# Kernel optimization log

Hardware: AMD Instinct MI355X
Metric: run time of the kernel (lower is better)

Reference implementation:

```python
import jax, jax.numpy as jnp
import numpy as np

B, M, N, D, NH, DH = 2, 2048, 2048, 1024, 16, 64
STD = 0.02

def setup_inputs() -> dict:
    key = jax.random.key(0)
    ks = jax.random.split(key, 7)
    query = jax.random.normal(ks[0], (B, M, D), dtype=jnp.float32)
    key_value = jax.random.normal(ks[1], (B, N, D), dtype=jnp.float32)
    key_padding_mask = jax.random.uniform(ks[2], (B, N)) < 0.1
    # torch Linear weight is (out,in); store as (in,out) for x @ W
    W_Q = STD * jax.random.truncated_normal(ks[3], -2.0, 2.0, (D, NH * DH), dtype=jnp.float32)
    W_K = STD * jax.random.truncated_normal(ks[4], -2.0, 2.0, (D, NH * DH), dtype=jnp.float32)
    W_V = STD * jax.random.truncated_normal(ks[5], -2.0, 2.0, (D, NH * DH), dtype=jnp.float32)
    W_O = STD * jax.random.truncated_normal(ks[6], -2.0, 2.0, (NH * DH, D), dtype=jnp.float32)
    return {"query": query, "key_value": key_value, "key_padding_mask": key_padding_mask,
            "W_Q": W_Q, "W_K": W_K, "W_V": W_V, "W_O": W_O}

def reference(query, key_value, key_padding_mask, W_Q, W_K, W_V, W_O):
    scale = 1.0 / jnp.sqrt(jnp.float32(DH))
    Q = (query @ W_Q).reshape(B, M, NH, DH)       # (B,M,H,dh)
    K = (key_value @ W_K).reshape(B, N, NH, DH)   # (B,N,H,dh)
    V = (key_value @ W_V).reshape(B, N, NH, DH)
    scores = jnp.einsum('bmhd,bnhd->bhmn', Q, K) * scale  # (B,H,M,N)
    scores = jnp.where(key_padding_mask[:, None, None, :], -jnp.inf, scores)
    attn = jax.nn.softmax(scores, axis=-1)
    out = jnp.einsum('bhmn,bnhd->bmhd', attn, V).reshape(B, M, NH * DH)
    return out @ W_O
```

## Files before the change

### kernel.cpp

```cpp
#include <hip/hip_runtime.h>
#include <math.h>

#define BB 2
#define SEQ 2048
#define DMODEL 1024
#define NHH 16
#define DHH 64

typedef __bf16 bf16;
typedef __attribute__((ext_vector_type(8))) __bf16 bf16x8;
typedef __attribute__((ext_vector_type(4))) float f32x4;

#define C1f 0.18033688011112042f
#define C2f -5.770780163555854f

__global__ __launch_bounds__(256) void cvt2_bf16(const float* __restrict__ in0,
                                                 bf16* __restrict__ out0,
                                                 const float* __restrict__ in1,
                                                 bf16* __restrict__ out1, int n8) {
  int i = blockIdx.x * 256 + threadIdx.x;
  if (i >= n8) return;
  const float* in = blockIdx.y ? in1 : in0;
  bf16* out = blockIdx.y ? out1 : out0;
  const float4* p = (const float4*)in + 2 * (size_t)i;
  float4 a = p[0], b = p[1];
  bf16x8 v;
  v[0] = (bf16)a.x; v[1] = (bf16)a.y; v[2] = (bf16)a.z; v[3] = (bf16)a.w;
  v[4] = (bf16)b.x; v[5] = (bf16)b.y; v[6] = (bf16)b.z; v[7] = (bf16)b.w;
  *((bf16x8*)out + i) = v;
}

__global__ __launch_bounds__(256) void wt_cvt(const float* __restrict__ W0, const float* __restrict__ W1,
                                              const float* __restrict__ W2, const float* __restrict__ W3,
                                              bf16* __restrict__ O0, bf16* __restrict__ O1,
                                              bf16* __restrict__ O2, bf16* __restrict__ O3) {
  __shared__ bf16 T[64][72];
  const float* W; bf16* O;
  switch (blockIdx.z) {
    case 0: W = W0; O = O0; break;
    case 1: W = W1; O = O1; break;
    case 2: W = W2; O = O2; break;
    default: W = W3; O = O3; break;
  }
  const int n0 = blockIdx.x * 64, k0 = blockIdx.y * 64;
  const int t = threadIdx.x;
  {
    int k = t >> 2, ns = (t & 3) * 16;
    const float* g = W + (size_t)(k0 + k) * DMODEL + n0 + ns;
#pragma unroll
    for (int q = 0; q < 4; ++q) {
      float4 f = *(const float4*)(g + 4 * q);
      T[ns + 4 * q + 0][k] = (bf16)f.x;
      T[ns + 4 * q + 1][k] = (bf16)f.y;
      T[ns + 4 * q + 2][k] = (bf16)f.z;
      T[ns + 4 * q + 3][k] = (bf16)f.w;
    }
  }
  __syncthreads();
  {
    int n = t >> 2, ks = (t & 3) * 16;
    bf16x8 a = *(const bf16x8*)&T[n][ks];
    bf16x8 b = *(const bf16x8*)&T[n][ks + 8];
    bf16* o = O + (size_t)(n0 + n) * DMODEL + k0 + ks;
    *(bf16x8*)o = a;
    *(bf16x8*)(o + 8) = b;
  }
}

template <bool F32OUT>
__device__ __forceinline__ void gemm64_body(const bf16* __restrict__ A,
                                            const bf16* __restrict__ Bt,
                                            float* __restrict__ Cf,
                                            bf16* __restrict__ Cb,
                                            bf16* As, bf16* Bs) {
  const int t = threadIdx.x;
  const int lane = t & 63, wave = t >> 6;
  const int l15 = lane & 15, quad = lane >> 4;
  const int bm = blockIdx.y * 64, bn = blockIdx.x * 128;
  const int wr = wave >> 1, wc = wave & 1;

  const int srow = t >> 3;
  const int slot = t & 7;
  const int schunk = slot ^ (srow & 7);
  const bf16* gA = A + (size_t)(bm + srow) * DMODEL + schunk * 8;
  const bf16* gB = Bt + (size_t)(bn + srow) * DMODEL + schunk * 8;
  const int soff = srow * 64 + slot * 8;

  bf16x8 areg[2][2], breg[2][4];
#pragma unroll
  for (int s = 0; s < 2; ++s) {
#pragma unroll
    for (int j = 0; j < 2; ++j)
      areg[s][j] = *(const bf16x8*)(gA + (size_t)(32 * j) * DMODEL + s * 64);
#pragma unroll
    for (int j = 0; j < 4; ++j)
      breg[s][j] = *(const bf16x8*)(gB + (size_t)(32 * j) * DMODEL + s * 64);
  }

  f32x4 acc[2][4] = {};

#pragma unroll
  for (int it = 0; it < 16; ++it) {
    const int sel = it & 1;
    __syncthreads();
#pragma unroll
    for (int j = 0; j < 2; ++j) *(bf16x8*)&As[j * 2048 + soff] = areg[sel][j];
#pragma unroll
    for (int j = 0; j < 4; ++j) *(bf16x8*)&Bs[j * 2048 + soff] = breg[sel][j];
    __syncthreads();
    if (it + 2 < 16) {
      const int kn = (it + 2) * 64;
#pragma unroll
      for (int j = 0; j < 2; ++j)
        areg[sel][j] = *(const bf16x8*)(gA + (size_t)(32 * j) * DMODEL + kn);
#pragma unroll
      for (int j = 0; j < 4; ++j)
        breg[sel][j] = *(const bf16x8*)(gB + (size_t)(32 * j) * DMODEL + kn);
    }
#pragma unroll
    for (int ks = 0; ks < 2; ++ks) {
      bf16x8 af[2], bfr[4];
#pragma unroll
      for (int mt = 0; mt < 2; ++mt) {
        int row = wr * 32 + mt * 16 + l15;
        int s = (ks * 4 + quad) ^ (row & 7);
        af[mt] = *(const bf16x8*)&As[row * 64 + s * 8];
      }
#pragma unroll
      for (int nt = 0; nt < 4; ++nt) {
        int row = wc * 64 + nt * 16 + l15;
        int s = (ks * 4 + quad) ^ (row & 7);
        bfr[nt] = *(const bf16x8*)&Bs[row * 64 + s * 8];
      }
#pragma unroll
      for (int mt = 0; mt < 2; ++mt)
#pragma unroll
        for (int nt = 0; nt < 4; ++nt)
          acc[mt][nt] = __builtin_amdgcn_mfma_f32_16x16x32_bf16(af[mt], bfr[nt], acc[mt][nt], 0, 0, 0);
    }
  }

#pragma unroll
  for (int mt = 0; mt < 2; ++mt)
#pragma unroll
    for (int nt = 0; nt < 4; ++nt)
#pragma unroll
      for (int r = 0; r < 4; ++r) {
        int row = bm + wr * 32 + mt * 16 + quad * 4 + r;
        int col = bn + wc * 64 + nt * 16 + l15;
        if (F32OUT) Cf[(size_t)row * DMODEL + col] = acc[mt][nt][r];
        else Cb[(size_t)row * DMODEL + col] = (bf16)acc[mt][nt][r];
      }
}

__global__ __launch_bounds__(256) void gemm_qkv(const bf16* __restrict__ qbf,
                                                const bf16* __restrict__ kvbf,
                                                const bf16* __restrict__ WtQ,
                                                const bf16* __restrict__ WtK,
                                                const bf16* __restrict__ WtV,
                                                bf16* __restrict__ Qb,
                                                bf16* __restrict__ Kb,
                                                bf16* __restrict__ Vb) {
  __shared__ bf16 As[64 * 64];
  __shared__ bf16 Bs[128 * 64];
  const bf16 *A, *Bt; bf16* C;
  switch (blockIdx.z) {
    case 0: A = qbf; Bt = WtQ; C = Qb; break;
    case 1: A = kvbf; Bt = WtK; C = Kb; break;
    default: A = kvbf; Bt = WtV; C = Vb; break;
  }
  gemm64_body<false>(A, Bt, nullptr, C, As, Bs);
}

__global__ __launch_bounds__(256) void gemm_out(const bf16* __restrict__ A,
                                                const bf16* __restrict__ Wt,
                                                float* __restrict__ C) {
  __shared__ bf16 As[64 * 64];
  __shared__ bf16 Bs[128 * 64];
  gemm64_body<true>(A, Wt, C, nullptr, As, Bs);
}

__global__ __launch_bounds__(256) void attn_mfma(const bf16* __restrict__ Qb,
                                                 const bf16* __restrict__ Kb,
                                                 const bf16* __restrict__ Vb,
                                                 const int* __restrict__ maskp,
                                                 bf16* __restrict__ Ob) {
  __shared__ bf16 Ks[2][64 * 64];
  __shared__ bf16 Vt[2][64][68];
  __shared__ bf16 Ps[4][32][36];
  __shared__ bf16 msk01[2][64];

  const int blk = blockIdx.x;
  const int h = blk & 15;
  const int b = (blk >> 4) & 1;
  const int qb = blk >> 5;
  const int t = threadIdx.x;
  const int wave = t >> 6, lane = t & 63;
  const int l15 = lane & 15, quad = lane >> 4;
  bf16(*PsW)[36] = Ps[wave];

  const int kr = t >> 2, kq = t & 3;
  const bf16* gK = Kb + (size_t)(b * SEQ + kr) * DMODEL + h * 64 + kq * 16;
  const int s0 = (kq * 2) ^ (kr & 7), s1 = (kq * 2 + 1) ^ (kr & 7);
  const int nv = (t & 31) * 2, dc = (t >> 5) * 8;
  const bf16* gV = Vb + (size_t)(b * SEQ + nv) * DMODEL + h * 64 + dc;
  const int* gM = maskp + b * SEQ;

  {
    bf16x8 k0 = *(const bf16x8*)(gK);
    bf16x8 k1 = *(const bf16x8*)(gK + 8);
    bf16x8 v0 = *(const bf16x8*)(gV);
    bf16x8 v1 = *(const bf16x8*)(gV + DMODEL);
    int2 m2 = *(const int2*)(gM + nv);
    *(bf16x8*)&Ks[0][kr * 64 + s0 * 8] = k0;
    *(bf16x8*)&Ks[0][kr * 64 + s1 * 8] = k1;
    union U { bf16x8 v; uint32_t dw[4]; } a, c;
    a.v = v0; c.v = v1;
    const uint32_t zA = m2.x ? 0u : 0xFFFFFFFFu;
    const uint32_t zB = m2.y ? 0u : 0xFFFFFFFFu;
#pragma unroll
    for (int d2 = 0; d2 < 4; ++d2) {
      uint32_t A0 = a.dw[d2] & zA, B0 = c.dw[d2] & zB;
      *(uint32_t*)&Vt[0][dc + 2 * d2 + 0][nv] = __builtin_amdgcn_perm(B0, A0, 0x05040100u);
      *(uint32_t*)&Vt[0][dc + 2 * d2 + 1][nv] = __builtin_amdgcn_perm(B0, A0, 0x07060302u);
    }
    if (t < 64) msk01[0][t] = gM[t] ? (bf16)0.f : (bf16)1.f;
  }

  bf16x8 qf[2][2];
#pragma unroll
  for (int mt = 0; mt < 2; ++mt)
#pragma unroll
    for (int ks = 0; ks < 2; ++ks) {
      const bf16* g = Qb + (size_t)(b * SEQ + qb * 128 + wave * 32 + mt * 16 + l15) * DMODEL +
                      h * 64 + ks * 32 + quad * 8;
      qf[mt][ks] = *(const bf16x8*)g;
    }

  f32x4 o[2][4] = {};
  f32x4 acc_l[2] = {};

  __syncthreads();

  for (int it = 0; it < SEQ / 64; ++it) {
    const int p = it & 1;
    const bool more = (it + 1) < SEQ / 64;
    bf16x8 kreg0, kreg1, vreg0, vreg1;
    int2 vm;
    int mreg = 0;
    if (more) {
      const int nn = (it + 1) * 64;
      const bf16* gK2 = gK + (size_t)nn * DMODEL;
      const bf16* gV2 = gV + (size_t)nn * DMODEL;
      kreg0 = *(const bf16x8*)(gK2);
      kreg1 = *(const bf16x8*)(gK2 + 8);
      vreg0 = *(const bf16x8*)(gV2);
      vreg1 = *(const bf16x8*)(gV2 + DMODEL);
      vm = *(const int2*)(gM + nn + nv);
      if (t < 64) mreg = gM[nn + t];
    }

    f32x4 s[2][4] = {};
#pragma unroll
    for (int ks = 0; ks < 2; ++ks) {
      bf16x8 kf[4];
#pragma unroll
      for (int nt = 0; nt < 4; ++nt) {
        int row = nt * 16 + l15;
        int sl = (ks * 4 + quad) ^ (row & 7);
        kf[nt] = *(const bf16x8*)&Ks[p][row * 64 + sl * 8];
      }
#pragma unroll
      for (int mt = 0; mt < 2; ++mt)
#pragma unroll
        for (int nt = 0; nt < 4; ++nt)
          s[mt][nt] = __builtin_amdgcn_mfma_f32_16x16x32_bf16(qf[mt][ks], kf[nt], s[mt][nt], 0, 0, 0);
    }

#pragma unroll
    for (int ks2 = 0; ks2 < 2; ++ks2) {
#pragma unroll
      for (int mt = 0; mt < 2; ++mt)
#pragma unroll
        for (int nt2 = 0; nt2 < 2; ++nt2)
#pragma unroll
          for (int r = 0; r < 4; ++r) {
            float pex = __builtin_amdgcn_exp2f(s[mt][ks2 * 2 + nt2][r] * C1f + C2f);
            PsW[mt * 16 + quad * 4 + r][nt2 * 16 + l15] = (bf16)pex;
          }
      bf16x8 pa[2], vb[4];
#pragma unroll
      for (int mt = 0; mt < 2; ++mt)
        pa[mt] = *(const bf16x8*)&PsW[mt * 16 + l15][quad * 8];
#pragma unroll
      for (int dt = 0; dt < 4; ++dt)
        vb[dt] = *(const bf16x8*)&Vt[p][dt * 16 + l15][ks2 * 32 + quad * 8];
      union OU { bf16x8 v; uint32_t dw[4]; } of;
      of.v = *(const bf16x8*)&msk01[p][ks2 * 32 + quad * 8];
      const uint32_t zc = (l15 == 0) ? 0xFFFFFFFFu : 0u;
#pragma unroll
      for (int d = 0; d < 4; ++d) of.dw[d] &= zc;
#pragma unroll
      for (int mt = 0; mt < 2; ++mt) {
#pragma unroll
        for (int dt = 0; dt < 4; ++dt)
          o[mt][dt] = __builtin_amdgcn_mfma_f32_16x16x32_bf16(pa[mt], vb[dt], o[mt][dt], 0, 0, 0);
        acc_l[mt] = __builtin_amdgcn_mfma_f32_16x16x32_bf16(pa[mt], of.v, acc_l[mt], 0, 0, 0);
      }
    }

    if (more) {
      const int q = 1 - p;
      *(bf16x8*)&Ks[q][kr * 64 + s0 * 8] = kreg0;
      *(bf16x8*)&Ks[q][kr * 64 + s1 * 8] = kreg1;
      union U { bf16x8 v; uint32_t dw[4]; } a, c;
      a.v = vreg0; c.v = vreg1;
      const uint32_t zA = vm.x ? 0u : 0xFFFFFFFFu;
      const uint32_t zB = vm.y ? 0u : 0xFFFFFFFFu;
#pragma unroll
      for (int d2 = 0; d2 < 4; ++d2) {
        uint32_t A0 = a.dw[d2] & zA, B0 = c.dw[d2] & zB;
        *(uint32_t*)&Vt[q][dc + 2 * d2 + 0][nv] = __builtin_amdgcn_perm(B0, A0, 0x05040100u);
        *(uint32_t*)&Vt[q][dc + 2 * d2 + 1][nv] = __builtin_amdgcn_perm(B0, A0, 0x07060302u);
      }
      if (t < 64) msk01[q][t] = mreg ? (bf16)0.f : (bf16)1.f;
    }
    __syncthreads();
  }

#pragma unroll
  for (int mt = 0; mt < 2; ++mt)
#pragma unroll
    for (int r = 0; r < 4; ++r) {
      float lv = __shfl(acc_l[mt][r], lane & 48);
      float inv = 1.f / lv;
      int row = b * SEQ + qb * 128 + wave * 32 + mt * 16 + quad * 4 + r;
#pragma unroll
      for (int dt = 0; dt < 4; ++dt) {
        int col = h * 64 + dt * 16 + l15;
        Ob[(size_t)row * DMODEL + col] = (bf16)(o[mt][dt][r] * inv);
      }
    }
}

extern "C" void kernel_launch(void* const* d_in, const int* in_sizes, int n_in,
                              void* d_out, int out_size, void* d_ws, size_t ws_size,
                              hipStream_t stream) {
  (void)in_sizes; (void)n_in; (void)out_size; (void)ws_size;
  const float* query = (const float*)d_in[0];
  const float* key_value = (const float*)d_in[1];
  const int* mask = (const int*)d_in[2];
  const float* W_Q = (const float*)d_in[3];
  const float* W_K = (const float*)d_in[4];
  const float* W_V = (const float*)d_in[5];
  const float* W_O = (const float*)d_in[6];
  float* out = (float*)d_out;

  const size_t TOK = (size_t)BB * SEQ;
  const size_t TE = TOK * DMODEL;
  char* w = (char*)d_ws;
  bf16* qbf = (bf16*)w;   w += TE * 2;
  bf16* kvbf = (bf16*)w;  w += TE * 2;
  bf16* WtQ = (bf16*)w;   w += (size_t)DMODEL * DMODEL * 2;
  bf16* WtK = (bf16*)w;   w += (size_t)DMODEL * DMODEL * 2;
  bf16* WtV = (bf16*)w;   w += (size_t)DMODEL * DMODEL * 2;
  bf16* WtO = (bf16*)w;   w += (size_t)DMODEL * DMODEL * 2;
  bf16* Qbuf = (bf16*)w;  w += TE * 2;
  bf16* Kbuf = (bf16*)w;  w += TE * 2;
  bf16* Vbuf = (bf16*)w;  w += TE * 2;
  bf16* Obuf = (bf16*)w;  w += TE * 2;

  cvt2_bf16<<<dim3(TE / 8 / 256, 2), 256, 0, stream>>>(query, qbf, key_value, kvbf, TE / 8);
  wt_cvt<<<dim3(16, 16, 4), 256, 0, stream>>>(W_Q, W_K, W_V, W_O, WtQ, WtK, WtV, WtO);

  gemm_qkv<<<dim3(DMODEL / 128, TOK / 64, 3), 256, 0, stream>>>(qbf, kvbf, WtQ, WtK, WtV,
                                                                Qbuf, Kbuf, Vbuf);

  attn_mfma<<<BB * NHH * (SEQ / 128), 256, 0, stream>>>(Qbuf, Kbuf, Vbuf, mask, Obuf);

  gemm_out<<<dim3(DMODEL / 128, TOK / 64), 256, 0, stream>>>(Obuf, WtO, out);
}
```

Baseline: 235.1 us.

## Use 8 waves per attention block, 16 query rows each, split K/V loading

The attention kernel now launches 512 threads per block instead of 256. Each of the 8 waves handles 16 query rows rather than 32, and the K-tile and V-tile prefetch work is split between the first four and last four waves. This roughly halves per-thread registers and work, aiming for more wave-level parallelism and better latency hiding. In exchange, every K/V tile loaded into LDS feeds half as many MFMAs per wave, and the larger block has more barrier overhead.

```diff
diff --git a/kernel.cpp b/kernel.cpp
--- a/kernel.cpp
+++ b/kernel.cpp
@@ -180,14 +180,14 @@
   gemm64_body<true>(A, Wt, C, nullptr, As, Bs);
 }
 
-__global__ __launch_bounds__(256) void attn_mfma(const bf16* __restrict__ Qb,
+__global__ __launch_bounds__(512) void attn_mfma(const bf16* __restrict__ Qb,
                                                  const bf16* __restrict__ Kb,
                                                  const bf16* __restrict__ Vb,
                                                  const int* __restrict__ maskp,
                                                  bf16* __restrict__ Ob) {
   __shared__ bf16 Ks[2][64 * 64];
   __shared__ bf16 Vt[2][64][68];
-  __shared__ bf16 Ps[4][32][36];
+  __shared__ bf16 Ps[8][16][36];
   __shared__ bf16 msk01[2][64];
 
   const int blk = blockIdx.x;
@@ -198,22 +198,26 @@
   const int wave = t >> 6, lane = t & 63;
   const int l15 = lane & 15, quad = lane >> 4;
   bf16(*PsW)[36] = Ps[wave];
-
-  const int kr = t >> 2, kq = t & 3;
+  const bool isK = wave < 4;
+  const int v2 = t & 255;
+
+  const int kr = v2 >> 2, kq = v2 & 3;
   const bf16* gK = Kb + (size_t)(b * SEQ + kr) * DMODEL + h * 64 + kq * 16;
   const int s0 = (kq * 2) ^ (kr & 7), s1 = (kq * 2 + 1) ^ (kr & 7);
-  const int nv = (t & 31) * 2, dc = (t >> 5) * 8;
+  const int nv = (v2 & 31) * 2, dc = (v2 >> 5) * 8;
   const bf16* gV = Vb + (size_t)(b * SEQ + nv) * DMODEL + h * 64 + dc;
   const int* gM = maskp + b * SEQ;
 
-  {
+  if (isK) {
     bf16x8 k0 = *(const bf16x8*)(gK);
     bf16x8 k1 = *(const bf16x8*)(gK + 8);
+    *(bf16x8*)&Ks[0][kr * 64 + s0 * 8] = k0;
+    *(bf16x8*)&Ks[0][kr * 64 + s1 * 8] = k1;
+    if (t < 64) msk01[0][t] = gM[t] ? (bf16)0.f : (bf16)1.f;
+  } else {
     bf16x8 v0 = *(const bf16x8*)(gV);
     bf16x8 v1 = *(const bf16x8*)(gV + DMODEL);
     int2 m2 = *(const int2*)(gM + nv);
-    *(bf16x8*)&Ks[0][kr * 64 + s0 * 8] = k0;
-    *(bf16x8*)&Ks[0][kr * 64 + s1 * 8] = k1;
     union U { bf16x8 v; uint32_t dw[4]; } a, c;
     a.v = v0; c.v = v1;
     const uint32_t zA = m2.x ? 0u : 0xFFFFFFFFu;
@@ -224,21 +228,18 @@
       *(uint32_t*)&Vt[0][dc + 2 * d2 + 0][nv] = __builtin_amdgcn_perm(B0, A0, 0x05040100u);
       *(uint32_t*)&Vt[0][dc + 2 * d2 + 1][nv] = __builtin_amdgcn_perm(B0, A0, 0x07060302u);
     }
-    if (t < 64) msk01[0][t] = gM[t] ? (bf16)0.f : (bf16)1.f;
-  }
-
-  bf16x8 qf[2][2];
-#pragma unroll
-  for (int mt = 0; mt < 2; ++mt)
-#pragma unroll
-    for (int ks = 0; ks < 2; ++ks) {
-      const bf16* g = Qb + (size_t)(b * SEQ + qb * 128 + wave * 32 + mt * 16 + l15) * DMODEL +
-                      h * 64 + ks * 32 + quad * 8;
-      qf[mt][ks] = *(const bf16x8*)g;
-    }
-
-  f32x4 o[2][4] = {};
-  f32x4 acc_l[2] = {};
+  }
+
+  bf16x8 qf[2];
+#pragma unroll
+  for (int ks = 0; ks < 2; ++ks) {
+    const bf16* g = Qb + (size_t)(b * SEQ + qb * 128 + wave * 16 + l15) * DMODEL +
+                    h * 64 + ks * 32 + quad * 8;
+    qf[ks] = *(const bf16x8*)g;
+  }
+
+  f32x4 o[4] = {};
+  f32x4 acc_l = {};
 
   __syncthreads();
 
@@ -250,17 +251,20 @@
     int mreg = 0;
     if (more) {
       const int nn = (it + 1) * 64;
-      const bf16* gK2 = gK + (size_t)nn * DMODEL;
-      const bf16* gV2 = gV + (size_t)nn * DMODEL;
-      kreg0 = *(const bf16x8*)(gK2);
-      kreg1 = *(const bf16x8*)(gK2 + 8);
-      vreg0 = *(const bf16x8*)(gV2);
-      vreg1 = *(const bf16x8*)(gV2 + DMODEL);
-      vm = *(const int2*)(gM + nn + nv);
-      if (t < 64) mreg = gM[nn + t];
-    }
-
-    f32x4 s[2][4] = {};
+      if (isK) {
+        const bf16* gK2 = gK + (size_t)nn * DMODEL;
+        kreg0 = *(const bf16x8*)(gK2);
+        kreg1 = *(const bf16x8*)(gK2 + 8);
+        if (t < 64) mreg = gM[nn + t];
+      } else {
+        const bf16* gV2 = gV + (size_t)nn * DMODEL;
+        vreg0 = *(const bf16x8*)(gV2);
+        vreg1 = *(const bf16x8*)(gV2 + DMODEL);
+        vm = *(const int2*)(gM + nn + nv);
+      }
+    }
+
+    f32x4 s[4] = {};
 #pragma unroll
     for (int ks = 0; ks < 2; ++ks) {
       bf16x8 kf[4];
@@ -271,27 +275,21 @@
         kf[nt] = *(const bf16x8*)&Ks[p][row * 64 + sl * 8];
       }
 #pragma unroll
-      for (int mt = 0; mt < 2; ++mt)
-#pragma unroll
-        for (int nt = 0; nt < 4; ++nt)
-          s[mt][nt] = __builtin_amdgcn_mfma_f32_16x16x32_bf16(qf[mt][ks], kf[nt], s[mt][nt], 0, 0, 0);
+      for (int nt = 0; nt < 4; ++nt)
+        s[nt] = __builtin_amdgcn_mfma_f32_16x16x32_bf16(qf[ks], kf[nt], s[nt], 0, 0, 0);
     }
 
 #pragma unroll
     for (int ks2 = 0; ks2 < 2; ++ks2) {
 #pragma unroll
-      for (int mt = 0; mt < 2; ++mt)
-#pragma unroll
-        for (int nt2 = 0; nt2 < 2; ++nt2)
-#pragma unroll
-          for (int r = 0; r < 4; ++r) {
-            float pex = __builtin_amdgcn_exp2f(s[mt][ks2 * 2 + nt2][r] * C1f + C2f);
-            PsW[mt * 16 + quad * 4 + r][nt2 * 16 + l15] = (bf16)pex;
-          }
-      bf16x8 pa[2], vb[4];
-#pragma unroll
-      for (int mt = 0; mt < 2; ++mt)
-        pa[mt] = *(const bf16x8*)&PsW[mt * 16 + l15][quad * 8];
+      for (int nt2 = 0; nt2 < 2; ++nt2)
+#pragma unroll
+        for (int r = 0; r < 4; ++r) {
+          float pex = __builtin_amdgcn_exp2f(s[ks2 * 2 + nt2][r] * C1f + C2f);
+          PsW[quad * 4 + r][nt2 * 16 + l15] = (bf16)pex;
+        }
+      bf16x8 pa, vb[4];
+      pa = *(const bf16x8*)&PsW[l15][quad * 8];
 #pragma unroll
       for (int dt = 0; dt < 4; ++dt)
         vb[dt] = *(const bf16x8*)&Vt[p][dt * 16 + l15][ks2 * 32 + quad * 8];
@@ -301,46 +299,44 @@
 #pragma unroll
       for (int d = 0; d < 4; ++d) of.dw[d] &= zc;
 #pragma unroll
-      for (int mt = 0; mt < 2; ++mt) {
-#pragma unroll
-        for (int dt = 0; dt < 4; ++dt)
-          o[mt][dt] = __builtin_amdgcn_mfma_f32_16x16x32_bf16(pa[mt], vb[dt], o[mt][dt], 0, 0, 0);
-        acc_l[mt] = __builtin_amdgcn_mfma_f32_16x16x32_bf16(pa[mt], of.v, acc_l[mt], 0, 0, 0);
-      }
+      for (int dt = 0; dt < 4; ++dt)
+        o[dt] = __builtin_amdgcn_mfma_f32_16x16x32_bf16(pa, vb[dt], o[dt], 0, 0, 0);
+      acc_l = __builtin_amdgcn_mfma_f32_16x16x32_bf16(pa, of.v, acc_l, 0, 0, 0);
     }
 
     if (more) {
       const int q = 1 - p;
-      *(bf16x8*)&Ks[q][kr * 64 + s0 * 8] = kreg0;
-      *(bf16x8*)&Ks[q][kr * 64 + s1 * 8] = kreg1;
-      union U { bf16x8 v; uint32_t dw[4]; } a, c;
-      a.v = vreg0; c.v = vreg1;
-      const uint32_t zA = vm.x ? 0u : 0xFFFFFFFFu;
-      const uint32_t zB = vm.y ? 0u : 0xFFFFFFFFu;
-#pragma unroll
-      for (int d2 = 0; d2 < 4; ++d2) {
-        uint32_t A0 = a.dw[d2] & zA, B0 = c.dw[d2] & zB;
-        *(uint32_t*)&Vt[q][dc + 2 * d2 + 0][nv] = __builtin_amdgcn_perm(B0, A0, 0x05040100u);
-        *(uint32_t*)&Vt[q][dc + 2 * d2 + 1][nv] = __builtin_amdgcn_perm(B0, A0, 0x07060302u);
-      }
-      if (t < 64) msk01[q][t] = mreg ? (bf16)0.f : (bf16)1.f;
+      if (isK) {
+        *(bf16x8*)&Ks[q][kr * 64 + s0 * 8] = kreg0;
+        *(bf16x8*)&Ks[q][kr * 64 + s1 * 8] = kreg1;
+        if (t < 64) msk01[q][t] = mreg ? (bf16)0.f : (bf16)1.f;
+      } else {
+        union U { bf16x8 v; uint32_t dw[4]; } a, c;
+        a.v = vreg0; c.v = vreg1;
+        const uint32_t zA = vm.x ? 0u : 0xFFFFFFFFu;
+        const uint32_t zB = vm.y ? 0u : 0xFFFFFFFFu;
+#pragma unroll
+        for (int d2 = 0; d2 < 4; ++d2) {
+          uint32_t A0 = a.dw[d2] & zA, B0 = c.dw[d2] & zB;
+          *(uint32_t*)&Vt[q][dc + 2 * d2 + 0][nv] = __builtin_amdgcn_perm(B0, A0, 0x05040100u);
+          *(uint32_t*)&Vt[q][dc + 2 * d2 + 1][nv] = __builtin_amdgcn_perm(B0, A0, 0x07060302u);
+        }
+      }
     }
     __syncthreads();
   }
 
 #pragma unroll
-  for (int mt = 0; mt < 2; ++mt)
-#pragma unroll
-    for (int r = 0; r < 4; ++r) {
-      float lv = __shfl(acc_l[mt][r], lane & 48);
-      float inv = 1.f / lv;
-      int row = b * SEQ + qb * 128 + wave * 32 + mt * 16 + quad * 4 + r;
-#pragma unroll
-      for (int dt = 0; dt < 4; ++dt) {
-        int col = h * 64 + dt * 16 + l15;
-        Ob[(size_t)row * DMODEL + col] = (bf16)(o[mt][dt][r] * inv);
-      }
-    }
+  for (int r = 0; r < 4; ++r) {
+    float lv = __shfl(acc_l[r], lane & 48);
+    float inv = 1.f / lv;
+    int row = b * SEQ + qb * 128 + wave * 16 + quad * 4 + r;
+#pragma unroll
+    for (int dt = 0; dt < 4; ++dt) {
+      int col = h * 64 + dt * 16 + l15;
+      Ob[(size_t)row * DMODEL + col] = (bf16)(o[dt][r] * inv);
+    }
+  }
 }
 
 extern "C" void kernel_launch(void* const* d_in, const int* in_sizes, int n_in,
@@ -376,7 +372,7 @@
   gemm_qkv<<<dim3(DMODEL / 128, TOK / 64, 3), 256, 0, stream>>>(qbf, kvbf, WtQ, WtK, WtV,
                                                                 Qbuf, Kbuf, Vbuf);
 
-  attn_mfma<<<BB * NHH * (SEQ / 128), 256, 0, stream>>>(Qbuf, Kbuf, Vbuf, mask, Obuf);
+  attn_mfma<<<BB * NHH * (SEQ / 128), 512, 0, stream>>>(Qbuf, Kbuf, Vbuf, mask, Obuf);
 
   gemm_out<<<dim3(DMODEL / 128, TOK / 64), 256, 0, stream>>>(Obuf, WtO, out);
 }
```

Measured after the change: 239.0 us. About the same (+1.7%).

## Use 128x128 GEMM tiles with direct global-to-LDS loads

Applied to the files above, without the earlier changes.

The projection GEMMs now use 128x128 output tiles with 4x4 MFMA accumulators per wave, and load A/B tiles straight into shared memory with global_load_lds instead of staging them through registers. This raises data reuse per tile and frees the registers that held prefetched tiles. It also drops the two-stage register double-buffering, so each k-step issues its load, waits at a barrier, computes, and waits again, which can expose memory latency. The grid halves in the M dimension, which lowers the block count per GEMM.

```diff
diff --git a/kernel.cpp b/kernel.cpp
--- a/kernel.cpp
+++ b/kernel.cpp
@@ -13,6 +13,12 @@
 
 #define C1f 0.18033688011112042f
 #define C2f -5.770780163555854f
+
+__device__ __forceinline__ void gl_lds16(const bf16* g, bf16* l) {
+  __builtin_amdgcn_global_load_lds(
+      (const __attribute__((address_space(1))) void*)g,
+      (__attribute__((address_space(3))) void*)l, 16, 0, 0);
+}
 
 __global__ __launch_bounds__(256) void cvt2_bf16(const float* __restrict__ in0,
                                                  bf16* __restrict__ out0,
@@ -68,61 +74,41 @@
 }
 
 template <bool F32OUT>
-__device__ __forceinline__ void gemm64_body(const bf16* __restrict__ A,
-                                            const bf16* __restrict__ Bt,
-                                            float* __restrict__ Cf,
-                                            bf16* __restrict__ Cb,
-                                            bf16* As, bf16* Bs) {
+__device__ __forceinline__ void gemm128_body(const bf16* __restrict__ A,
+                                             const bf16* __restrict__ Bt,
+                                             float* __restrict__ Cf,
+                                             bf16* __restrict__ Cb,
+                                             bf16* As, bf16* Bs) {
   const int t = threadIdx.x;
   const int lane = t & 63, wave = t >> 6;
   const int l15 = lane & 15, quad = lane >> 4;
-  const int bm = blockIdx.y * 64, bn = blockIdx.x * 128;
+  const int bm = blockIdx.y * 128, bn = blockIdx.x * 128;
   const int wr = wave >> 1, wc = wave & 1;
 
-  const int srow = t >> 3;
-  const int slot = t & 7;
-  const int schunk = slot ^ (srow & 7);
-  const bf16* gA = A + (size_t)(bm + srow) * DMODEL + schunk * 8;
-  const bf16* gB = Bt + (size_t)(bn + srow) * DMODEL + schunk * 8;
-  const int soff = srow * 64 + slot * 8;
-
-  bf16x8 areg[2][2], breg[2][4];
-#pragma unroll
-  for (int s = 0; s < 2; ++s) {
-#pragma unroll
-    for (int j = 0; j < 2; ++j)
-      areg[s][j] = *(const bf16x8*)(gA + (size_t)(32 * j) * DMODEL + s * 64);
-#pragma unroll
-    for (int j = 0; j < 4; ++j)
-      breg[s][j] = *(const bf16x8*)(gB + (size_t)(32 * j) * DMODEL + s * 64);
-  }
-
-  f32x4 acc[2][4] = {};
-
-#pragma unroll
-  for (int it = 0; it < 16; ++it) {
-    const int sel = it & 1;
+  const int srow = wave * 32 + (lane >> 3);
+  const int sc = lane & 7;
+  const int ca = sc ^ ((lane >> 3) & 7);
+  const bf16* gA = A + (size_t)(bm + srow) * DMODEL + ca * 8;
+  const bf16* gB = Bt + (size_t)(bn + srow) * DMODEL + ca * 8;
+  bf16* lA = &As[wave * 32 * 64];
+  bf16* lB = &Bs[wave * 32 * 64];
+
+  f32x4 acc[4][4] = {};
+
+  for (int kt = 0; kt < DMODEL / 64; ++kt) {
+    const int kk = kt * 64;
+#pragma unroll
+    for (int j = 0; j < 4; ++j) {
+      gl_lds16(gA + (size_t)(j * 8) * DMODEL + kk, lA + j * 8 * 64);
+      gl_lds16(gB + (size_t)(j * 8) * DMODEL + kk, lB + j * 8 * 64);
+    }
     __syncthreads();
 #pragma unroll
-    for (int j = 0; j < 2; ++j) *(bf16x8*)&As[j * 2048 + soff] = areg[sel][j];
-#pragma unroll
-    for (int j = 0; j < 4; ++j) *(bf16x8*)&Bs[j * 2048 + soff] = breg[sel][j];
-    __syncthreads();
-    if (it + 2 < 16) {
-      const int kn = (it + 2) * 64;
-#pragma unroll
-      for (int j = 0; j < 2; ++j)
-        areg[sel][j] = *(const bf16x8*)(gA + (size_t)(32 * j) * DMODEL + kn);
-#pragma unroll
-      for (int j = 0; j < 4; ++j)
-        breg[sel][j] = *(const bf16x8*)(gB + (size_t)(32 * j) * DMODEL + kn);
-    }
-#pragma unroll
     for (int ks = 0; ks < 2; ++ks) {
-      bf16x8 af[2], bfr[4];
-#pragma unroll
-      for (int mt = 0; mt < 2; ++mt) {
-        int row = wr * 32 + mt * 16 + l15;
+      bf16x8 af[4], bfr[4];
+#pragma unroll
+      for (int mt = 0; mt < 4; ++mt) {
+        int row = wr * 64 + mt * 16 + l15;
         int s = (ks * 4 + quad) ^ (row & 7);
         af[mt] = *(const bf16x8*)&As[row * 64 + s * 8];
       }
@@ -133,20 +119,21 @@
         bfr[nt] = *(const bf16x8*)&Bs[row * 64 + s * 8];
       }
 #pragma unroll
-      for (int mt = 0; mt < 2; ++mt)
+      for (int mt = 0; mt < 4; ++mt)
 #pragma unroll
         for (int nt = 0; nt < 4; ++nt)
           acc[mt][nt] = __builtin_amdgcn_mfma_f32_16x16x32_bf16(af[mt], bfr[nt], acc[mt][nt], 0, 0, 0);
     }
-  }
-
-#pragma unroll
-  for (int mt = 0; mt < 2; ++mt)
+    __syncthreads();
+  }
+
+#pragma unroll
+  for (int mt = 0; mt < 4; ++mt)
 #pragma unroll
     for (int nt = 0; nt < 4; ++nt)
 #pragma unroll
       for (int r = 0; r < 4; ++r) {
-        int row = bm + wr * 32 + mt * 16 + quad * 4 + r;
+        int row = bm + wr * 64 + mt * 16 + quad * 4 + r;
         int col = bn + wc * 64 + nt * 16 + l15;
         if (F32OUT) Cf[(size_t)row * DMODEL + col] = acc[mt][nt][r];
         else Cb[(size_t)row * DMODEL + col] = (bf16)acc[mt][nt][r];
@@ -161,7 +148,7 @@
                                                 bf16* __restrict__ Qb,
                                                 bf16* __restrict__ Kb,
                                                 bf16* __restrict__ Vb) {
-  __shared__ bf16 As[64 * 64];
+  __shared__ bf16 As[128 * 64];
   __shared__ bf16 Bs[128 * 64];
   const bf16 *A, *Bt; bf16* C;
   switch (blockIdx.z) {
@@ -169,15 +156,15 @@
     case 1: A = kvbf; Bt = WtK; C = Kb; break;
     default: A = kvbf; Bt = WtV; C = Vb; break;
   }
-  gemm64_body<false>(A, Bt, nullptr, C, As, Bs);
+  gemm128_body<false>(A, Bt, nullptr, C, As, Bs);
 }
 
 __global__ __launch_bounds__(256) void gemm_out(const bf16* __restrict__ A,
                                                 const bf16* __restrict__ Wt,
                                                 float* __restrict__ C) {
-  __shared__ bf16 As[64 * 64];
+  __shared__ bf16 As[128 * 64];
   __shared__ bf16 Bs[128 * 64];
-  gemm64_body<true>(A, Wt, C, nullptr, As, Bs);
+  gemm128_body<true>(A, Wt, C, nullptr, As, Bs);
 }
 
 __global__ __launch_bounds__(256) void attn_mfma(const bf16* __restrict__ Qb,
@@ -373,10 +360,10 @@
   cvt2_bf16<<<dim3(TE / 8 / 256, 2), 256, 0, stream>>>(query, qbf, key_value, kvbf, TE / 8);
   wt_cvt<<<dim3(16, 16, 4), 256, 0, stream>>>(W_Q, W_K, W_V, W_O, WtQ, WtK, WtV, WtO);
 
-  gemm_qkv<<<dim3(DMODEL / 128, TOK / 64, 3), 256, 0, stream>>>(qbf, kvbf, WtQ, WtK, WtV,
-                                                                Qbuf, Kbuf, Vbuf);
+  gemm_qkv<<<dim3(DMODEL / 128, TOK / 128, 3), 256, 0, stream>>>(qbf, kvbf, WtQ, WtK, WtV,
+                                                                 Qbuf, Kbuf, Vbuf);
 
   attn_mfma<<<BB * NHH * (SEQ / 128), 256, 0, stream>>>(Qbuf, Kbuf, Vbuf, mask, Obuf);
 
-  gemm_out<<<dim3(DMODEL / 128, TOK / 64), 256, 0, stream>>>(Obuf, WtO, out);
-}
+  gemm_out<<<dim3(DMODEL / 128, TOK / 128), 256, 0, stream>>>(Obuf, WtO, out);
+}
```

After: 240.5 us. 2.3% more time.
